# Kernel tuning notes

Measured on AMD Instinct MI355X. Metric: run time of the kernel, lower is better.

The kernel has to match this reference:

```python
import jax, jax.numpy as jnp
import numpy as np

D_MODEL = 768
NUM_HEADS = 12
SEGMENT_LENGTHS = (2048, 4096, 8192)
DILATION_RATES = (1, 2, 4)
LN_EPS = 1e-5


def setup_inputs() -> dict:
    key = jax.random.key(0)
    ks = jax.random.split(key, 8)
    b, n, dm = 2, 8192, D_MODEL
    s = 1.0 / np.sqrt(dm)
    return {
        "x": jax.random.normal(ks[0], (b, n, dm), dtype=jnp.float32),
        "w_in": jax.random.normal(ks[1], (dm, dm), dtype=jnp.float32) * s,
        "b_in": jnp.zeros((dm,), dtype=jnp.float32),
        "w_out": jax.random.normal(ks[2], (dm, dm), dtype=jnp.float32) * s,
        "b_out": jnp.zeros((dm,), dtype=jnp.float32),
        "ln_gamma": jnp.ones((dm,), dtype=jnp.float32),
        "ln_beta": jnp.zeros((dm,), dtype=jnp.float32),
    }


def _dilated_attention(q, k, v):
    # q, k, v: (b, n, h, d)
    b, n, h, d = q.shape
    num_groups = len(DILATION_RATES)
    group_sizes = [h // num_groups] * num_groups
    for i in range(h % num_groups):
        group_sizes[i] += 1
    scale = 1.0 / jnp.sqrt(jnp.asarray(d, q.dtype))
    out = jnp.zeros_like(q)
    for i, (g, r, s) in enumerate(zip(group_sizes, DILATION_RATES, SEGMENT_LENGTHS)):
        offset = i % r
        hmin, hmax = i * g, (i + 1) * g
        nseg = n // s
        def slc(t):
            # (b, nseg, s, h, d) -> strided dilation slice + head group slice
            return t.reshape(b, nseg, s, h, d)[:, :, offset::r, hmin:hmax, :]
        qs, ks_, vs = slc(q), slc(k), slc(v)  # (b, nseg, se, g, d), se = s // r
        attn = jnp.einsum('bnqhd,bnkhd->bnhqk', qs, ks_) * scale
        attn = jax.nn.softmax(attn, axis=-1)
        x = jnp.einsum('bnhqk,bnkhd->bnqhd', attn, vs)  # (b, nseg, se, g, d)
        # renormalize by sum over (segment, within-segment) dims, as in source
        x = x / x.sum(axis=(1, 2), keepdims=True)
        out = (out.reshape(b, nseg, s, h, d)
                  .at[:, :, offset::r, hmin:hmax, :].add(x)
                  .reshape(b, n, h, d))
    return out / num_groups


def reference(x, w_in, b_in, w_out, b_out, ln_gamma, ln_beta):
    b, n, dm = x.shape
    hd = dm // NUM_HEADS
    # QKVProjectionOption.SAME: q = k = v = proj(x)
    q = x @ w_in.T + b_in
    qh = q.reshape(b, n, NUM_HEADS, hd)
    o = _dilated_attention(qh, qh, qh)
    o = o.reshape(b, n, dm)
    mu = o.mean(axis=-1, keepdims=True)
    var = ((o - mu) ** 2).mean(axis=-1, keepdims=True)
    o = (o - mu) / jnp.sqrt(var + LN_EPS) * ln_gamma + ln_beta
    return o @ w_out.T + b_out
```

## Files before the change

kernel.cpp:

```cpp
#include <hip/hip_runtime.h>
#include <hip/hip_bf16.h>
#include <math.h>

#define B_   2
#define N_   8192
#define DM   768
#define NH   12
#define HD   64

#define QL_ELEM_OFF 12582912ull
#define AC_OFF      12582912ull
#define SUMS_OFF    19922944ull

typedef short bf16x8 __attribute__((ext_vector_type(8)));
typedef _Float16 f16x8 __attribute__((ext_vector_type(8)));
typedef _Float16 f16x4 __attribute__((ext_vector_type(4)));
typedef float f32x4  __attribute__((ext_vector_type(4)));

__device__ __forceinline__ size_t ac_base(int grp) {
    return 8388608ull - (8388608ull >> grp);
}

__device__ __forceinline__ unsigned short f2bf(float f) {
    __hip_bfloat16 h = __float2bfloat16(f);
    return __builtin_bit_cast(unsigned short, h);
}
__device__ __forceinline__ float bf2f(unsigned short u) {
    __hip_bfloat16 h = __builtin_bit_cast(__hip_bfloat16, u);
    return __bfloat162float(h);
}
__device__ __forceinline__ void split2h(float f, _Float16& h, _Float16& l) {
    h = (_Float16)f;
    l = (_Float16)(f - (float)h);
}

#define SW(row, col) ((((row) << 6)) + ((((col) >> 3) ^ ((row) & 7)) << 3) + ((col) & 7))

__global__ __launch_bounds__(256) void gemm_mfma_split(
    const float* __restrict__ A, const float* __restrict__ W,
    const float* __restrict__ bias, float* __restrict__ C,
    _Float16* __restrict__ Ch, _Float16* __restrict__ Cl) {
    __shared__ unsigned short AsH[128][40];
    __shared__ unsigned short AsL[128][40];
    __shared__ unsigned short WsH[128][40];
    __shared__ unsigned short WsL[128][40];

    const int t    = threadIdx.x;
    const int lane = t & 63;
    const int wv   = t >> 6;
    const int c    = lane & 15, q = lane >> 4;
    const int mw   = (wv & 1) * 64, nw = (wv >> 1) * 64;
    const int m0   = blockIdx.x * 128, n0 = blockIdx.y * 128;

    const int srow = t >> 1;
    const int scol = (t & 1) * 16;
    const float* ap = A + (size_t)(m0 + srow) * DM + scol;
    const float* wp = W + (size_t)(n0 + srow) * DM + scol;

    f32x4 acc[4][4];
#pragma unroll
    for (int mi = 0; mi < 4; ++mi)
#pragma unroll
        for (int ni = 0; ni < 4; ++ni) {
            acc[mi][ni][0] = 0.f; acc[mi][ni][1] = 0.f;
            acc[mi][ni][2] = 0.f; acc[mi][ni][3] = 0.f;
        }

    for (int k0 = 0; k0 < DM; k0 += 32) {
        float av[16], wvv[16];
        *(float4*)&av[0]  = *(const float4*)(ap + k0);
        *(float4*)&av[4]  = *(const float4*)(ap + k0 + 4);
        *(float4*)&av[8]  = *(const float4*)(ap + k0 + 8);
        *(float4*)&av[12] = *(const float4*)(ap + k0 + 12);
        *(float4*)&wvv[0]  = *(const float4*)(wp + k0);
        *(float4*)&wvv[4]  = *(const float4*)(wp + k0 + 4);
        *(float4*)&wvv[8]  = *(const float4*)(wp + k0 + 8);
        *(float4*)&wvv[12] = *(const float4*)(wp + k0 + 12);
        __syncthreads();
#pragma unroll
        for (int i = 0; i < 16; ++i) {
            const float x = av[i];
            const unsigned short xh = f2bf(x);
            AsH[srow][scol + i] = xh;
            AsL[srow][scol + i] = f2bf(x - bf2f(xh));
            const float y = wvv[i];
            const unsigned short yh = f2bf(y);
            WsH[srow][scol + i] = yh;
            WsL[srow][scol + i] = f2bf(y - bf2f(yh));
        }
        __syncthreads();

        bf16x8 ah[4], al[4], bh[4], bl[4];
#pragma unroll
        for (int i = 0; i < 4; ++i) {
            ah[i] = *(const bf16x8*)&AsH[mw + i*16 + c][q*8];
            al[i] = *(const bf16x8*)&AsL[mw + i*16 + c][q*8];
            bh[i] = *(const bf16x8*)&WsH[nw + i*16 + c][q*8];
            bl[i] = *(const bf16x8*)&WsL[nw + i*16 + c][q*8];
        }
#pragma unroll
        for (int mi = 0; mi < 4; ++mi)
#pragma unroll
            for (int ni = 0; ni < 4; ++ni) {
                f32x4 v = acc[mi][ni];
                v = __builtin_amdgcn_mfma_f32_16x16x32_bf16(ah[mi], bl[ni], v, 0, 0, 0);
                v = __builtin_amdgcn_mfma_f32_16x16x32_bf16(al[mi], bh[ni], v, 0, 0, 0);
                v = __builtin_amdgcn_mfma_f32_16x16x32_bf16(ah[mi], bh[ni], v, 0, 0, 0);
                acc[mi][ni] = v;
            }
    }

#pragma unroll
    for (int ni = 0; ni < 4; ++ni) {
        const int col = n0 + nw + ni*16 + c;
        const float bv = bias[col];
#pragma unroll
        for (int mi = 0; mi < 4; ++mi)
#pragma unroll
            for (int r = 0; r < 4; ++r) {
                const int row = m0 + mw + mi*16 + q*4 + r;
                const float val = acc[mi][ni][r] + bv;
                if (Ch) {
                    _Float16 hh, ll;
                    split2h(val, hh, ll);
                    Ch[(size_t)row * DM + col] = hh;
                    Cl[(size_t)row * DM + col] = ll;
                } else {
                    C[(size_t)row * DM + col] = val;
                }
            }
    }
}

__global__ __launch_bounds__(256, 2) void attn_mfma_kernel(
    const _Float16* __restrict__ Qh, const _Float16* __restrict__ Ql,
    float* __restrict__ AC) {
    __shared__ __align__(16) _Float16 KH[4096],  KL[4096];
    __shared__ __align__(16) _Float16 VTH[4096], VTL[4096];
    __shared__ __align__(16) _Float16 PTH[8192], PTL[8192];

    const int t    = threadIdx.x;
    const int lane = t & 63;
    const int w    = t >> 6;
    const int c    = lane & 15, quad = lane >> 4;

    const int bi  = blockIdx.x;
    const int qt  = bi & 15;
    const int bsh = bi >> 4;
    int grp, local;
    if (bsh < 32)      { grp = 0; local = bsh; }
    else if (bsh < 48) { grp = 1; local = bsh - 32; }
    else               { grp = 2; local = bsh - 48; }
    const int nseg = 4 >> grp;
    const int sseg = 2048 << grp;
    const int r    = 1 << grp;
    const int b    = local / (nseg * 4);
    const int rem  = local - b * nseg * 4;
    const int seg  = rem >> 2;
    const int hg   = rem & 3;
    const int head = grp * 4 + hg;

    const size_t row0 = (size_t)(b * N_ + seg * sseg + grp);
    const int hoff = head * HD;

    const int r0 = (t >> 4) * 4;
    const int c0 = (t & 15) * 4;

    f16x8 qfh[2][2], qfl[2][2];
#pragma unroll
    for (int jt = 0; jt < 2; ++jt) {
        const int qrow = qt*128 + w*32 + jt*16 + c;
        const size_t qoff = (row0 + (size_t)qrow * r) * DM + hoff;
#pragma unroll
        for (int kc = 0; kc < 2; ++kc) {
            f16x8 h = *(const f16x8*)(Qh + qoff + kc*32 + quad*8);
            f16x8 l = *(const f16x8*)(Ql + qoff + kc*32 + quad*8);
            qfh[jt][kc] = h * (_Float16)0.125f;
            qfl[jt][kc] = l * (_Float16)0.125f;
        }
    }

    {
        f16x4 hh[4], ll[4];
#pragma unroll
        for (int i = 0; i < 4; ++i) {
            const size_t off = (row0 + (size_t)(r0 + i) * r) * DM + hoff + c0;
            hh[i] = *(const f16x4*)(Qh + off);
            ll[i] = *(const f16x4*)(Ql + off);
        }
#pragma unroll
        for (int i = 0; i < 4; ++i) {
            *(f16x4*)&KH[SW(r0 + i, c0)] = hh[i];
            *(f16x4*)&KL[SW(r0 + i, c0)] = ll[i];
        }
#pragma unroll
        for (int j = 0; j < 4; ++j) {
            *(f16x4*)&VTH[SW(c0 + j, r0)] = (f16x4){hh[0][j], hh[1][j], hh[2][j], hh[3][j]};
            *(f16x4*)&VTL[SW(c0 + j, r0)] = (f16x4){ll[0][j], ll[1][j], ll[2][j], ll[3][j]};
        }
    }
    __syncthreads();

    float m_st[2] = {-1e30f, -1e30f};
    float l_st[2] = {0.f, 0.f};
    f32x4 o[2][4];
#pragma unroll
    for (int jt = 0; jt < 2; ++jt)
#pragma unroll
        for (int i = 0; i < 4; ++i) {
            o[jt][i][0] = 0.f; o[jt][i][1] = 0.f;
            o[jt][i][2] = 0.f; o[jt][i][3] = 0.f;
        }

    for (int kt = 0; kt < 32; ++kt) {
        f16x4 nh[4], nl[4];
        if (kt < 31) {
#pragma unroll
            for (int i = 0; i < 4; ++i) {
                const size_t off = (row0 + (size_t)((kt+1)*64 + r0 + i) * r) * DM + hoff + c0;
                nh[i] = *(const f16x4*)(Qh + off);
                nl[i] = *(const f16x4*)(Ql + off);
            }
        }

        f32x4 s[2][4];
#pragma unroll
        for (int jt = 0; jt < 2; ++jt)
#pragma unroll
            for (int mt = 0; mt < 4; ++mt) {
                s[jt][mt][0] = 0.f; s[jt][mt][1] = 0.f;
                s[jt][mt][2] = 0.f; s[jt][mt][3] = 0.f;
            }
#pragma unroll
        for (int kc = 0; kc < 2; ++kc)
#pragma unroll
            for (int mt = 0; mt < 4; ++mt) {
                f16x8 ah = *(const f16x8*)&KH[SW(mt*16 + c, kc*32 + quad*8)];
                f16x8 al = *(const f16x8*)&KL[SW(mt*16 + c, kc*32 + quad*8)];
#pragma unroll
                for (int jt = 0; jt < 2; ++jt) {
                    f32x4 v = s[jt][mt];
                    v = __builtin_amdgcn_mfma_f32_16x16x32_f16(ah, qfl[jt][kc], v, 0, 0, 0);
                    v = __builtin_amdgcn_mfma_f32_16x16x32_f16(al, qfh[jt][kc], v, 0, 0, 0);
                    v = __builtin_amdgcn_mfma_f32_16x16x32_f16(ah, qfh[jt][kc], v, 0, 0, 0);
                    s[jt][mt] = v;
                }
            }

#pragma unroll
        for (int jt = 0; jt < 2; ++jt) {
            float mloc = s[jt][0][0];
#pragma unroll
            for (int mt = 0; mt < 4; ++mt)
#pragma unroll
                for (int rg = 0; rg < 4; ++rg) mloc = fmaxf(mloc, s[jt][mt][rg]);
            mloc = fmaxf(mloc, __shfl_xor(mloc, 16));
            mloc = fmaxf(mloc, __shfl_xor(mloc, 32));
            const float mnew  = fmaxf(m_st[jt], mloc);
            const float alpha = __expf(m_st[jt] - mnew);
            m_st[jt] = mnew;

            float psum = 0.f;
            const int prow = w*32 + jt*16 + c;
#pragma unroll
            for (int mt = 0; mt < 4; ++mt) {
                f16x4 hh, ll;
#pragma unroll
                for (int rg = 0; rg < 4; ++rg) {
                    const float pv = __expf(s[jt][mt][rg] - mnew);
                    psum += pv;
                    _Float16 th, tl;
                    split2h(pv, th, tl);
                    hh[rg] = th;
                    ll[rg] = tl;
                }
                *(f16x4*)&PTH[SW(prow, mt*16 + quad*4)] = hh;
                *(f16x4*)&PTL[SW(prow, mt*16 + quad*4)] = ll;
            }
            psum += __shfl_xor(psum, 16);
            psum += __shfl_xor(psum, 32);
            l_st[jt] = l_st[jt] * alpha + psum;
#pragma unroll
            for (int mtd = 0; mtd < 4; ++mtd) {
                o[jt][mtd][0] *= alpha; o[jt][mtd][1] *= alpha;
                o[jt][mtd][2] *= alpha; o[jt][mtd][3] *= alpha;
            }
        }

#pragma unroll
        for (int kc = 0; kc < 2; ++kc) {
            f16x8 ph[2], pl[2];
#pragma unroll
            for (int jt = 0; jt < 2; ++jt) {
                ph[jt] = *(const f16x8*)&PTH[SW(w*32 + jt*16 + c, kc*32 + quad*8)];
                pl[jt] = *(const f16x8*)&PTL[SW(w*32 + jt*16 + c, kc*32 + quad*8)];
            }
#pragma unroll
            for (int mtd = 0; mtd < 4; ++mtd) {
                f16x8 vh = *(const f16x8*)&VTH[SW(mtd*16 + c, kc*32 + quad*8)];
                f16x8 vl = *(const f16x8*)&VTL[SW(mtd*16 + c, kc*32 + quad*8)];
#pragma unroll
                for (int jt = 0; jt < 2; ++jt) {
                    f32x4 v = o[jt][mtd];
                    v = __builtin_amdgcn_mfma_f32_16x16x32_f16(vh, pl[jt], v, 0, 0, 0);
                    v = __builtin_amdgcn_mfma_f32_16x16x32_f16(vl, ph[jt], v, 0, 0, 0);
                    v = __builtin_amdgcn_mfma_f32_16x16x32_f16(vh, ph[jt], v, 0, 0, 0);
                    o[jt][mtd] = v;
                }
            }
        }

        if (kt < 31) {
            __syncthreads();
#pragma unroll
            for (int i = 0; i < 4; ++i) {
                *(f16x4*)&KH[SW(r0 + i, c0)] = nh[i];
                *(f16x4*)&KL[SW(r0 + i, c0)] = nl[i];
            }
#pragma unroll
            for (int j = 0; j < 4; ++j) {
                *(f16x4*)&VTH[SW(c0 + j, r0)] = (f16x4){nh[0][j], nh[1][j], nh[2][j], nh[3][j]};
                *(f16x4*)&VTL[SW(c0 + j, r0)] = (f16x4){nl[0][j], nl[1][j], nl[2][j], nl[3][j]};
            }
            __syncthreads();
        }
    }

    const size_t gbase = ac_base(grp);
#pragma unroll
    for (int jt = 0; jt < 2; ++jt) {
        const float inv = 1.0f / l_st[jt];
        const int qrow = qt*128 + w*32 + jt*16 + c;
        float* dst = AC + gbase + ((size_t)((b*nseg + seg)*2048 + qrow)) * 256 + hg*64;
#pragma unroll
        for (int mtd = 0; mtd < 4; ++mtd) {
            float4 v = make_float4(o[jt][mtd][0]*inv, o[jt][mtd][1]*inv,
                                   o[jt][mtd][2]*inv, o[jt][mtd][3]*inv);
            *(float4*)(dst + mtd*16 + quad*4) = v;
        }
    }
}

__global__ __launch_bounds__(256) void sum_kernel(
    const float* __restrict__ AC, float* __restrict__ SUMS) {
    const int bi = blockIdx.x;
    int grp, local;
    if (bi < 64)      { grp = 0; local = bi; }
    else if (bi < 96) { grp = 1; local = bi - 64; }
    else              { grp = 2; local = bi - 96; }
    const int chunks = 32 >> grp;
    const int b  = local / chunks;
    const int ch = local - b * chunks;
    const int P  = 8192 >> grp;
    const size_t base = ac_base(grp) + ((size_t)b * P + ch * 256) * 256 + threadIdx.x;
    float acc = 0.f;
    for (int p = 0; p < 256; ++p) acc += AC[base + (size_t)p * 256];
    atomicAdd(&SUMS[((grp << 1) + b) * 256 + threadIdx.x], acc);
}

__device__ __forceinline__ float block_reduce_sum(float val, float* sdata) {
    __syncthreads();
#pragma unroll
    for (int o = 32; o > 0; o >>= 1) val += __shfl_down(val, o);
    const int lane = threadIdx.x & 63, wid = threadIdx.x >> 6;
    if (lane == 0) sdata[wid] = val;
    __syncthreads();
    return sdata[0] + sdata[1] + sdata[2] + sdata[3];
}

__global__ __launch_bounds__(256) void renorm_ln_kernel(
    const float* __restrict__ AC, const float* __restrict__ SUMS,
    const float* __restrict__ gamma, const float* __restrict__ beta,
    float* __restrict__ OLN) {
    __shared__ float sdata[4];
    const int pos = blockIdx.x;
    const int b = pos >> 13;
    const int n = pos & 8191;

    float v[3];
    int dms[3];
#pragma unroll
    for (int jj = 0; jj < 3; ++jj) {
        const int dm = threadIdx.x + (jj << 8);
        dms[jj] = dm;
        const int h = dm >> 6, d = dm & 63;
        const int grp = h >> 2, hg = h & 3;
        const int r = 1 << grp;
        const int p = n & ((2048 << grp) - 1);
        float val = 0.f;
        if ((p & (r - 1)) == grp) {
            const int nseg = 4 >> grp;
            const int seg  = n >> (11 + grp);
            const int j    = (p - grp) >> grp;
            const float s  = SUMS[((grp << 1) + b) * 256 + (hg << 6) + d];
            val = AC[ac_base(grp) + ((size_t)((b*nseg + seg)*2048 + j)) * 256 + (hg << 6) + d]
                  / (3.0f * s);
        }
        v[jj] = val;
    }

    const float tot = block_reduce_sum(v[0] + v[1] + v[2], sdata);
    const float mu  = tot * (1.0f / 768.0f);
    float sq = 0.f;
#pragma unroll
    for (int jj = 0; jj < 3; ++jj) {
        const float d0 = v[jj] - mu;
        sq += d0 * d0;
    }
    const float var  = block_reduce_sum(sq, sdata) * (1.0f / 768.0f);
    const float rstd = rsqrtf(var + 1e-5f);

    float* dst = OLN + (size_t)pos * 768;
#pragma unroll
    for (int jj = 0; jj < 3; ++jj)
        dst[dms[jj]] = (v[jj] - mu) * rstd * gamma[dms[jj]] + beta[dms[jj]];
}

extern "C" void kernel_launch(void* const* d_in, const int* in_sizes, int n_in,
                              void* d_out, int out_size, void* d_ws, size_t ws_size,
                              hipStream_t stream) {
    const float* x     = (const float*)d_in[0];
    const float* w_in  = (const float*)d_in[1];
    const float* b_in  = (const float*)d_in[2];
    const float* w_out = (const float*)d_in[3];
    const float* b_out = (const float*)d_in[4];
    const float* gamma = (const float*)d_in[5];
    const float* beta  = (const float*)d_in[6];
    float* out = (float*)d_out;

    float* ws   = (float*)d_ws;
    _Float16* Qh = (_Float16*)ws;
    _Float16* Ql = (_Float16*)ws + QL_ELEM_OFF;
    float* AC   = ws + AC_OFF;
    float* SUMS = ws + SUMS_OFF;
    float* OLN  = ws;

    gemm_mfma_split<<<dim3(128, 6), 256, 0, stream>>>(x, w_in, b_in, nullptr, Qh, Ql);
    attn_mfma_kernel<<<896, 256, 0, stream>>>(Qh, Ql, AC);
    (void)hipMemsetAsync(SUMS, 0, 1536 * sizeof(float), stream);
    sum_kernel<<<112, 256, 0, stream>>>(AC, SUMS);
    renorm_ln_kernel<<<B_ * N_, 256, 0, stream>>>(AC, SUMS, gamma, beta, OLN);
    gemm_mfma_split<<<dim3(128, 6), 256, 0, stream>>>(OLN, w_out, b_out, out,
                                                      nullptr, nullptr);
}
```

Baseline: 569.7 us.

## Keep softmax P in registers via lane shuffles, drop LDS P buffers

Removes the PTH/PTL shared-memory staging of the softmax probabilities and builds the PV MFMA operand fragments directly from registers with cross-lane shuffles. This cuts LDS use enough to raise launch bounds to 4 blocks per CU. It also adds a second XOR term to the V-transpose swizzle to reduce bank conflicts, and skips the rescale of the accumulator when no lane's running max increases. In exchange there is more register pressure under the tighter launch bound and extra shuffle instructions per tile.

```diff
diff --git a/kernel.cpp b/kernel.cpp
--- a/kernel.cpp
+++ b/kernel.cpp
@@ -35,6 +35,7 @@
 }
 
 #define SW(row, col) ((((row) << 6)) + ((((col) >> 3) ^ ((row) & 7)) << 3) + ((col) & 7))
+#define SWV(row, col) ((((row) << 6)) + ((((col) >> 3) ^ ((row) & 7) ^ (((row) >> 3) & 7)) << 3) + ((col) & 7))
 
 __global__ __launch_bounds__(256) void gemm_mfma_split(
     const float* __restrict__ A, const float* __restrict__ W,
@@ -132,12 +133,37 @@
     }
 }
 
-__global__ __launch_bounds__(256, 2) void attn_mfma_kernel(
+__device__ __forceinline__ f16x4 shfl_xor_h4(f16x4 v, int mask) {
+    int2 u = __builtin_bit_cast(int2, v);
+    u.x = __shfl_xor(u.x, mask);
+    u.y = __shfl_xor(u.y, mask);
+    return __builtin_bit_cast(f16x4, u);
+}
+
+__device__ __forceinline__ f16x8 build_pfrag(f16x4 p0, f16x4 p1, int quad) {
+    const bool hi_half = (quad >> 1) != 0;
+    const bool odd     = (quad & 1) != 0;
+    f16x4 S1 = hi_half ? p1 : p0;
+    f16x4 S2 = hi_half ? p0 : p1;
+    f16x4 R1  = shfl_xor_h4(S1, 16);
+    f16x4 A32 = shfl_xor_h4(S2, 32);
+    f16x4 A48 = shfl_xor_h4(S2, 48);
+    f16x4 f1lo = odd ? R1  : S1,  f1hi = odd ? S1  : R1;
+    f16x4 f3lo = odd ? A48 : A32, f3hi = odd ? A32 : A48;
+    const bool useF1 = (quad == 0) || (quad == 3);
+    f16x4 lo = useF1 ? f1lo : f3lo;
+    f16x4 hi = useF1 ? f1hi : f3hi;
+    f16x8 r;
+    r[0] = lo[0]; r[1] = lo[1]; r[2] = lo[2]; r[3] = lo[3];
+    r[4] = hi[0]; r[5] = hi[1]; r[6] = hi[2]; r[7] = hi[3];
+    return r;
+}
+
+__global__ __launch_bounds__(256, 4) void attn_mfma_kernel(
     const _Float16* __restrict__ Qh, const _Float16* __restrict__ Ql,
     float* __restrict__ AC) {
     __shared__ __align__(16) _Float16 KH[4096],  KL[4096];
     __shared__ __align__(16) _Float16 VTH[4096], VTL[4096];
-    __shared__ __align__(16) _Float16 PTH[8192], PTL[8192];
 
     const int t    = threadIdx.x;
     const int lane = t & 63;
@@ -195,8 +221,8 @@
         }
 #pragma unroll
         for (int j = 0; j < 4; ++j) {
-            *(f16x4*)&VTH[SW(c0 + j, r0)] = (f16x4){hh[0][j], hh[1][j], hh[2][j], hh[3][j]};
-            *(f16x4*)&VTL[SW(c0 + j, r0)] = (f16x4){ll[0][j], ll[1][j], ll[2][j], ll[3][j]};
+            *(f16x4*)&VTH[SWV(c0 + j, r0)] = (f16x4){hh[0][j], hh[1][j], hh[2][j], hh[3][j]};
+            *(f16x4*)&VTL[SWV(c0 + j, r0)] = (f16x4){ll[0][j], ll[1][j], ll[2][j], ll[3][j]};
         }
     }
     __syncthreads();
@@ -247,6 +273,7 @@
                 }
             }
 
+        f16x4 ph_[2][4], pl_[2][4];
 #pragma unroll
         for (int jt = 0; jt < 2; ++jt) {
             float mloc = s[jt][0][0];
@@ -256,55 +283,57 @@
                 for (int rg = 0; rg < 4; ++rg) mloc = fmaxf(mloc, s[jt][mt][rg]);
             mloc = fmaxf(mloc, __shfl_xor(mloc, 16));
             mloc = fmaxf(mloc, __shfl_xor(mloc, 32));
-            const float mnew  = fmaxf(m_st[jt], mloc);
-            const float alpha = __expf(m_st[jt] - mnew);
-            m_st[jt] = mnew;
-
+            if (!__all(mloc <= m_st[jt])) {
+                const float mnew  = fmaxf(m_st[jt], mloc);
+                const float alpha = __expf(m_st[jt] - mnew);
+                m_st[jt] = mnew;
+                l_st[jt] *= alpha;
+#pragma unroll
+                for (int mtd = 0; mtd < 4; ++mtd) {
+                    o[jt][mtd][0] *= alpha; o[jt][mtd][1] *= alpha;
+                    o[jt][mtd][2] *= alpha; o[jt][mtd][3] *= alpha;
+                }
+            }
+            const float mcur = m_st[jt];
             float psum = 0.f;
-            const int prow = w*32 + jt*16 + c;
 #pragma unroll
             for (int mt = 0; mt < 4; ++mt) {
                 f16x4 hh, ll;
 #pragma unroll
                 for (int rg = 0; rg < 4; ++rg) {
-                    const float pv = __expf(s[jt][mt][rg] - mnew);
+                    const float pv = __expf(s[jt][mt][rg] - mcur);
                     psum += pv;
                     _Float16 th, tl;
                     split2h(pv, th, tl);
                     hh[rg] = th;
                     ll[rg] = tl;
                 }
-                *(f16x4*)&PTH[SW(prow, mt*16 + quad*4)] = hh;
-                *(f16x4*)&PTL[SW(prow, mt*16 + quad*4)] = ll;
+                ph_[jt][mt] = hh;
+                pl_[jt][mt] = ll;
             }
             psum += __shfl_xor(psum, 16);
             psum += __shfl_xor(psum, 32);
-            l_st[jt] = l_st[jt] * alpha + psum;
+            l_st[jt] += psum;
+        }
+
+#pragma unroll
+        for (int kc = 0; kc < 2; ++kc) {
+            f16x8 pbh[2], pbl[2];
+#pragma unroll
+            for (int jt = 0; jt < 2; ++jt) {
+                pbh[jt] = build_pfrag(ph_[jt][2*kc], ph_[jt][2*kc + 1], quad);
+                pbl[jt] = build_pfrag(pl_[jt][2*kc], pl_[jt][2*kc + 1], quad);
+            }
 #pragma unroll
             for (int mtd = 0; mtd < 4; ++mtd) {
-                o[jt][mtd][0] *= alpha; o[jt][mtd][1] *= alpha;
-                o[jt][mtd][2] *= alpha; o[jt][mtd][3] *= alpha;
-            }
-        }
-
-#pragma unroll
-        for (int kc = 0; kc < 2; ++kc) {
-            f16x8 ph[2], pl[2];
-#pragma unroll
-            for (int jt = 0; jt < 2; ++jt) {
-                ph[jt] = *(const f16x8*)&PTH[SW(w*32 + jt*16 + c, kc*32 + quad*8)];
-                pl[jt] = *(const f16x8*)&PTL[SW(w*32 + jt*16 + c, kc*32 + quad*8)];
-            }
-#pragma unroll
-            for (int mtd = 0; mtd < 4; ++mtd) {
-                f16x8 vh = *(const f16x8*)&VTH[SW(mtd*16 + c, kc*32 + quad*8)];
-                f16x8 vl = *(const f16x8*)&VTL[SW(mtd*16 + c, kc*32 + quad*8)];
+                f16x8 vh = *(const f16x8*)&VTH[SWV(mtd*16 + c, kc*32 + quad*8)];
+                f16x8 vl = *(const f16x8*)&VTL[SWV(mtd*16 + c, kc*32 + quad*8)];
 #pragma unroll
                 for (int jt = 0; jt < 2; ++jt) {
                     f32x4 v = o[jt][mtd];
-                    v = __builtin_amdgcn_mfma_f32_16x16x32_f16(vh, pl[jt], v, 0, 0, 0);
-                    v = __builtin_amdgcn_mfma_f32_16x16x32_f16(vl, ph[jt], v, 0, 0, 0);
-                    v = __builtin_amdgcn_mfma_f32_16x16x32_f16(vh, ph[jt], v, 0, 0, 0);
+                    v = __builtin_amdgcn_mfma_f32_16x16x32_f16(vh, pbl[jt], v, 0, 0, 0);
+                    v = __builtin_amdgcn_mfma_f32_16x16x32_f16(vl, pbh[jt], v, 0, 0, 0);
+                    v = __builtin_amdgcn_mfma_f32_16x16x32_f16(vh, pbh[jt], v, 0, 0, 0);
                     o[jt][mtd] = v;
                 }
             }
@@ -319,8 +348,8 @@
             }
 #pragma unroll
             for (int j = 0; j < 4; ++j) {
-                *(f16x4*)&VTH[SW(c0 + j, r0)] = (f16x4){nh[0][j], nh[1][j], nh[2][j], nh[3][j]};
-                *(f16x4*)&VTL[SW(c0 + j, r0)] = (f16x4){nl[0][j], nl[1][j], nl[2][j], nl[3][j]};
+                *(f16x4*)&VTH[SWV(c0 + j, r0)] = (f16x4){nh[0][j], nh[1][j], nh[2][j], nh[3][j]};
+                *(f16x4*)&VTL[SWV(c0 + j, r0)] = (f16x4){nl[0][j], nl[1][j], nl[2][j], nl[3][j]};
             }
             __syncthreads();
         }
```

After: 758.7 us. 1.33x slower.
